# Performance work log

Measured on AMD Instinct MI355X. Metric: run time of the kernel, lower is better.

Reference implementation:

```python
import jax, jax.numpy as jnp
import numpy as np

EPS = 1e-6
E_LAMBDA = 1e-4
HID = 128


def conv1d_same(z, w, b):
    # z: [B,C,S], w: [O,I,K] -> [B,O,S]
    out = jax.lax.conv_general_dilated(z, w, window_strides=(1,), padding='SAME',
                                       dimension_numbers=('NCH', 'OIH', 'NCH'))
    return out + b[None, :, None]


def queue_layer(x, k_s, k_a):
    dist = x[:, :, -3]
    air = x[:, :, -5]
    E_S = k_s * dist + EPS
    lam = k_a / (air + EPS)
    rho = jnp.minimum(lam * E_S, 0.99)  # torch.clamp(max=0.99)
    W_q = rho / (1.0 - rho + EPS) * E_S
    Wn = (W_q - W_q.min()) / (W_q.max() - W_q.min() + EPS)
    L_q = lam * W_q
    Ln = (L_q - L_q.min()) / (L_q.max() - L_q.min() + EPS)
    return Wn[..., None], Ln[..., None]  # [B,S,1] each


def simam(z, d, l):
    # z: [B,C,S]; d,l: [B,1,1]
    mu = z.mean(axis=2, keepdims=True)
    e = ((z - mu) ** 2).mean(axis=2, keepdims=True) + d + 0.5 * l + E_LAMBDA
    return z * jax.nn.sigmoid(e)


def mogrifier_lstm(seq, d_seq, lq_seq, mod_w, mod_b, w_ih, w_hh, b_ih, b_hh):
    # seq: [B,S,C]; d_seq,lq_seq: [B,S,1]
    B = seq.shape[0]
    h0 = jnp.zeros((B, HID), seq.dtype)
    c0 = jnp.zeros((B, HID), seq.dtype)
    xs = (jnp.swapaxes(seq, 0, 1), jnp.swapaxes(d_seq, 0, 1), jnp.swapaxes(lq_seq, 0, 1))

    def step(carry, xt):
        h, c = carry
        s_t, d_t, l_t = xt
        gate_in = jnp.concatenate([h, d_t, l_t], axis=1)  # [B, H+2]
        m = jax.nn.sigmoid(gate_in @ mod_w.T + mod_b)      # [B, C]
        g = (m * s_t) @ w_ih.T + b_ih + h @ w_hh.T + b_hh  # [B, 4H]
        i, f, gg, o = jnp.split(g, 4, axis=1)              # torch LSTMCell gate order
        c = jax.nn.sigmoid(f) * c + jax.nn.sigmoid(i) * jnp.tanh(gg)
        h = jax.nn.sigmoid(o) * jnp.tanh(c)
        return (h, c), None

    (h, _), _ = jax.lax.scan(step, (h0, c0), xs)
    return h


def setup_inputs() -> dict:
    key = jax.random.key(0)
    ks = jax.random.split(key, 16)
    s = 0.02
    B, S, F = 256, 512, 16
    C1, C2, C3, H, NC = 64, 128, 256, HID, 8
    inp = {
        'x': jax.random.uniform(ks[0], (B, S, F), dtype=jnp.float32),
        'k_s': jnp.float32(1.0),
        'k_a': jnp.float32(1.0),
        'w1': jax.random.normal(ks[1], (C1, F, 3), jnp.float32) * s,
        'b1': jnp.zeros((C1,), jnp.float32),
        'w2': jax.random.normal(ks[2], (C2, C1, 3), jnp.float32) * s,
        'b2': jnp.zeros((C2,), jnp.float32),
        'w3': jax.random.normal(ks[3], (C3, C2, 3), jnp.float32) * s,
        'b3': jnp.zeros((C3,), jnp.float32),
        'mod_w': jax.random.normal(ks[4], (C3, H + 2), jnp.float32) * s,
        'mod_b': jnp.zeros((C3,), jnp.float32),
        'w_ih': jax.random.normal(ks[5], (4 * H, C3), jnp.float32) * s,
        'w_hh': jax.random.normal(ks[6], (4 * H, H), jnp.float32) * s,
        'b_ih': jnp.zeros((4 * H,), jnp.float32),
        'b_hh': jnp.zeros((4 * H,), jnp.float32),
        'cls_w': jax.random.normal(ks[7], (NC, H), jnp.float32) * s,
        'cls_b': jnp.zeros((NC,), jnp.float32),
    }
    return inp


def reference(x, k_s, k_a, w1, b1, w2, b2, w3, b3, mod_w, mod_b,
              w_ih, w_hh, b_ih, b_hh, cls_w, cls_b):
    d_seq, lq_seq = queue_layer(x, k_s, k_a)       # [B,S,1] each
    d = d_seq.mean(axis=1, keepdims=True).transpose(0, 2, 1)   # [B,1,1]
    l = lq_seq.mean(axis=1, keepdims=True).transpose(0, 2, 1)  # [B,1,1]
    z = x.transpose(0, 2, 1)                       # [B,F,S]
    for w, b in ((w1, b1), (w2, b2), (w3, b3)):
        z = simam(jax.nn.relu(conv1d_same(z, w, b)), d, l)
    z = z.transpose(0, 2, 1)                       # [B,S,C3]
    h_last = mogrifier_lstm(z, d_seq, lq_seq, mod_w, mod_b, w_ih, w_hh, b_ih, b_hh)
    return h_last @ cls_w.T + cls_b                # [B,num_classes]
```

## Files before the change

kernel.cpp:

```cpp
#include <hip/hip_runtime.h>
#include <hip/hip_fp16.h>
#include <cstdint>

#define EPSQ 1e-6f
#define E_LAM 1e-4f

#define B_ 256
#define S_ 512
#define F_ 16
#define C1_ 64
#define C2_ 128
#define C3_ 256
#define HID_ 128

typedef _Float16 f16x8 __attribute__((ext_vector_type(8)));
typedef _Float16 f16x4 __attribute__((ext_vector_type(4)));
typedef float f32x4 __attribute__((ext_vector_type(4)));

__device__ __forceinline__ float sigm(float x){
  return __builtin_amdgcn_rcpf(1.0f + __builtin_amdgcn_exp2f(-1.44269504f*x));
}
__device__ __forceinline__ float tanhft(float x){
  float e = __builtin_amdgcn_exp2f(-2.88539008f*x);
  return (1.0f - e) * __builtin_amdgcn_rcpf(1.0f + e);
}

#define PINV(x) asm volatile("" : "+v"(reinterpret_cast<f32x4&>(x)))

__global__ void k_init(unsigned int* mm){
  int t = threadIdx.x;
  if (t < 4) mm[t] = (t & 1) ? 0u : 0x7f800000u;
}

__global__ __launch_bounds__(256) void k_queue1(
    const float* __restrict__ x, const float* __restrict__ ksp, const float* __restrict__ kap,
    float* __restrict__ Wq, float* __restrict__ Lq, unsigned int* __restrict__ mm){
  int i = blockIdx.x * 256 + threadIdx.x;
  float ks = ksp[0], ka = kap[0];
  float dist = x[(size_t)i*F_ + 13];
  float air  = x[(size_t)i*F_ + 11];
  float ES  = ks*dist + EPSQ;
  float lam = ka/(air + EPSQ);
  float rho = fminf(lam*ES, 0.99f);
  float wq  = rho/(1.0f - rho + EPSQ)*ES;
  float lq  = lam*wq;
  Wq[i] = wq; Lq[i] = lq;
  float wmin=wq, wmax=wq, lmin=lq, lmax=lq;
  for (int o=32;o;o>>=1){
    wmin = fminf(wmin, __shfl_xor(wmin,o));
    wmax = fmaxf(wmax, __shfl_xor(wmax,o));
    lmin = fminf(lmin, __shfl_xor(lmin,o));
    lmax = fmaxf(lmax, __shfl_xor(lmax,o));
  }
  if ((threadIdx.x & 63) == 0){
    atomicMin(mm+0, __float_as_uint(wmin));
    atomicMax(mm+1, __float_as_uint(wmax));
    atomicMin(mm+2, __float_as_uint(lmin));
    atomicMax(mm+3, __float_as_uint(lmax));
  }
}

__global__ __launch_bounds__(256) void k_queue2(
    float* __restrict__ Wq, float* __restrict__ Lq, const unsigned int* __restrict__ mm,
    float* __restrict__ dbar, float* __restrict__ lbar){
  int b = blockIdx.x, t = threadIdx.x;
  float minW = __uint_as_float(mm[0]), maxW = __uint_as_float(mm[1]);
  float minL = __uint_as_float(mm[2]), maxL = __uint_as_float(mm[3]);
  float dW = maxW - minW + EPSQ;
  float dL = maxL - minL + EPSQ;
  float sw = 0.f, sl = 0.f;
  for (int s=t; s<S_; s+=256){
    size_t idx = (size_t)b*S_ + s;
    float wn = (Wq[idx]-minW)/dW;
    float ln = (Lq[idx]-minL)/dL;
    Wq[idx]=wn; Lq[idx]=ln;
    sw += wn; sl += ln;
  }
  for (int o=32;o;o>>=1){ sw += __shfl_xor(sw,o); sl += __shfl_xor(sl,o); }
  __shared__ float rs[4], rl[4];
  int w = t>>6;
  if ((t&63)==0){ rs[w]=sw; rl[w]=sl; }
  __syncthreads();
  if (t==0){
    dbar[b] = (rs[0]+rs[1]+rs[2]+rs[3]) * (1.0f/S_);
    lbar[b] = (rl[0]+rl[1]+rl[2]+rl[3]) * (1.0f/S_);
  }
}

__global__ void k_repack_conv(const float* __restrict__ w, float* __restrict__ wr, int CIN, int COUT){
  int idx = blockIdx.x*256 + threadIdx.x;
  int N = CIN*COUT*3;
  if (idx >= N) return;
  int co = idx % COUT;
  int r  = idx / COUT;
  int k  = r % 3;
  int ci = r / 3;
  wr[idx] = w[((size_t)co*CIN + ci)*3 + k];
}

__global__ void k_repack_w3f(const float* __restrict__ w3, __half* __restrict__ W3f){
  int idx = blockIdx.x*256 + threadIdx.x;
  if (idx >= 98304) return;
  int f = idx & 7, l = (idx>>3) & 63, t = idx >> 9;
  int kb = t % 12, nt = t / 12;
  int co = nt*16 + (l&15);
  int K  = kb*32 + ((l>>4)<<3) + f;
  int kidx = K >> 7, ci = K & 127;
  W3f[idx] = __float2half(w3[((size_t)co*C2_ + ci)*3 + kidx]);
}

__global__ void k_repack_frags(
    const float* __restrict__ mod_w, const float* __restrict__ w_ih, const float* __restrict__ w_hh,
    const float* __restrict__ b_ih, const float* __restrict__ b_hh, const float* __restrict__ mod_b,
    __half* __restrict__ WIHf, __half* __restrict__ WHHf, __half* __restrict__ MWf,
    float* __restrict__ BG){
  int idx = blockIdx.x*256 + threadIdx.x;
  const int NIH = 32*8*512;
  const int NHH = 32*4*512;
  const int NMW = 16*5*512;
  if (idx < NIH){
    int f = idx & 7, l = (idx>>3)&63; int t = idx>>9; int kk = t & 7; int nt = t>>3;
    int row = nt*16 + (l&15), k = kk*32 + ((l>>4)<<3) + f;
    WIHf[idx] = __float2half(w_ih[(size_t)row*256 + k]);
  } else if (idx < NIH+NHH){
    int j = idx - NIH;
    int f = j&7, l = (j>>3)&63; int t = j>>9; int kk = t&3; int nt = t>>2;
    int row = nt*16 + (l&15), k = kk*32 + ((l>>4)<<3) + f;
    WHHf[j] = __float2half(w_hh[(size_t)row*128 + k]);
  } else if (idx < NIH+NHH+NMW){
    int j = idx - NIH - NHH;
    int f = j&7, l = (j>>3)&63; int t = j>>9; int kk = t%5; int nt = t/5;
    int row = nt*16 + (l&15), k = kk*32 + ((l>>4)<<3) + f;
    float v = (k < 130) ? mod_w[(size_t)row*130 + k] : ((k == 130) ? mod_b[row] : 0.0f);
    MWf[j] = __float2half(v);
  } else if (idx < NIH+NHH+NMW+512){
    int k = idx - NIH-NHH-NMW;
    BG[k] = b_ih[k] + b_hh[k];
  }
}

template<int CIN, int COUT, int TOUT>
__global__ __launch_bounds__(256) void k_conv(
    const float* __restrict__ in, const float* __restrict__ wr,
    const float* __restrict__ bias, float* __restrict__ out){
  constexpr int SG    = 256/COUT;
  constexpr int STILE = SG*8;
  constexpr int RS    = STILE+4;
  __shared__ __align__(16) float lds[CIN*RS];
  int b = blockIdx.y;
  int s_base = blockIdx.x * STILE;
  int tid = threadIdx.x;
  for (int idx=tid; idx<CIN*(STILE+2); idx+=256){
    int ci = idx & (F_-1);
    int sp = idx >> 4;
    int sg = s_base - 1 + sp;
    float v = (sg>=0 && sg<S_) ? in[((size_t)b*S_+sg)*F_ + ci] : 0.0f;
    lds[ci*RS+sp] = v;
  }
  __syncthreads();
  int co = tid % COUT;
  int sg = tid / COUT;
  int s0 = sg*8;
  float acc[8] = {0,0,0,0,0,0,0,0};
  for (int ci=0; ci<CIN; ci++){
    const float* w = &wr[(ci*3)*COUT + co];
    float w0=w[0], w1=w[COUT], w2=w[2*COUT];
    const float* r = &lds[ci*RS + s0];
    float4 va = *(const float4*)(r);
    float4 vb = *(const float4*)(r+4);
    float2 vc = *(const float2*)(r+8);
    float v[10] = {va.x,va.y,va.z,va.w, vb.x,vb.y,vb.z,vb.w, vc.x,vc.y};
    #pragma unroll
    for (int ss=0; ss<8; ss++) acc[ss] += w0*v[ss] + w1*v[ss+1] + w2*v[ss+2];
  }
  float bb = bias[co];
  float* o = &out[((size_t)b*COUT+co)*S_ + s_base + s0];
  float4 o0 = make_float4(fmaxf(acc[0]+bb,0.f), fmaxf(acc[1]+bb,0.f), fmaxf(acc[2]+bb,0.f), fmaxf(acc[3]+bb,0.f));
  float4 o1 = make_float4(fmaxf(acc[4]+bb,0.f), fmaxf(acc[5]+bb,0.f), fmaxf(acc[6]+bb,0.f), fmaxf(acc[7]+bb,0.f));
  *(float4*)(o)   = o0;
  *(float4*)(o+4) = o1;
}

template<int CIN, int COUT, int TOUT>
__global__ __launch_bounds__(256) void k_cgemm(
    const float* __restrict__ in, const float* __restrict__ wr,
    const float* __restrict__ bias, const float* __restrict__ gate,
    float* __restrict__ out){
  constexpr int TS   = 64;
  constexpr int RS   = 72;
  constexpr int SPT  = COUT/32;
  constexpr int NCG  = COUT/8;
  constexpr int KC   = (CIN == 64) ? 8 : 4;
  constexpr int WROW = NCG*10;
  __shared__ __align__(16) float sIn[CIN*RS];
  __shared__ __align__(16) float sW[3*KC*WROW];
  int b = blockIdx.y;
  int s_base = blockIdx.x * TS;
  int tid = threadIdx.x;
  for (int idx = tid; idx < CIN*(TS+2); idx += 256){
    int ci = idx / (TS+2), sp = idx % (TS+2);
    int sg = s_base - 1 + sp;
    float v = (sg>=0 && sg<S_) ? in[((size_t)b*CIN+ci)*S_ + sg] : 0.0f;
    sIn[ci*RS + sp] = v * gate[b*CIN + ci];
  }
  int cg = tid % NCG, sg2 = tid / NCG;
  int co0 = cg*8, s0 = sg2*SPT;
  float2 acc[8][SPT/2] = {};
  for (int ci0 = 0; ci0 < CIN; ci0 += KC){
    __syncthreads();
    for (int e = tid; e < 3*KC*COUT; e += 256){
      int krow = e / COUT, co = e % COUT;
      sW[krow*WROW + (co>>3)*10 + (co&7)] = wr[(size_t)3*ci0*COUT + e];
    }
    __syncthreads();
    #pragma unroll
    for (int cii = 0; cii < KC; cii++){
      const float* rp = &sIn[(ci0+cii)*RS + s0];
      float win[SPT+4];
      #pragma unroll
      for (int j = 0; j < (SPT+4)/4; j++)
        *(float4*)&win[4*j] = *(const float4*)(rp + 4*j);
      #pragma unroll
      for (int kidx = 0; kidx < 3; kidx++){
        const float* wrow = &sW[(cii*3 + kidx)*WROW + cg*10];
        float ws[8];
        *(float2*)&ws[0] = *(const float2*)(wrow);
        *(float2*)&ws[2] = *(const float2*)(wrow+2);
        *(float2*)&ws[4] = *(const float2*)(wrow+4);
        *(float2*)&ws[6] = *(const float2*)(wrow+6);
        #pragma unroll
        for (int i = 0; i < 8; i++){
          #pragma unroll
          for (int j = 0; j < SPT/2; j++){
            acc[i][j].x += ws[i]*win[2*j+kidx];
            acc[i][j].y += ws[i]*win[2*j+1+kidx];
          }
        }
      }
    }
  }
  float bs[8];
  *(float4*)&bs[0] = *(const float4*)(bias+co0);
  *(float4*)&bs[4] = *(const float4*)(bias+co0+4);
  #pragma unroll
  for (int i=0;i<8;i++){
    float v[SPT];
    #pragma unroll
    for (int j=0;j<SPT;j++){
      float a = (j&1) ? acc[i][j>>1].y : acc[i][j>>1].x;
      v[j] = fmaxf(a + bs[i], 0.0f);
    }
    float* op = &out[((size_t)b*COUT+co0+i)*S_ + s_base+s0];
    #pragma unroll
    for (int j4=0;j4<SPT;j4+=4) *(float4*)(op+j4) = *(float4*)&v[j4];
  }
}

__global__ __launch_bounds__(256) void k_cmfma3(
    const float* __restrict__ z2, const __half* __restrict__ W3f,
    const float* __restrict__ bias, const float* __restrict__ gate,
    float* __restrict__ out){
  __shared__ __align__(16) _Float16 zT[66*128];
  int b = blockIdx.y;
  int s_base = blockIdx.x * 64;
  int tid = threadIdx.x;
  const int lane = tid & 63, w = tid >> 6;
  for (int idx = tid; idx < 128*66; idx += 256){
    int ci = idx / 66, j = idx % 66;
    int sg = s_base + j - 1;
    float v = (sg >= 0 && sg < S_) ? z2[((size_t)b*C2_ + ci)*S_ + sg] * gate[b*C2_ + ci] : 0.0f;
    *(_Float16*)((char*)zT + ((j*256 + ci*2) ^ ((j&7)<<4))) = (_Float16)v;
  }
  __syncthreads();
  f32x4 acc[4][4];
  float bv[4];
  #pragma unroll
  for (int i=0;i<4;i++) bv[i] = bias[(w*4+i)*16 + (lane&15)];
  #pragma unroll
  for (int ts=0;ts<4;ts++)
    #pragma unroll
    for (int i=0;i<4;i++) acc[ts][i] = (f32x4){bv[i],bv[i],bv[i],bv[i]};

  const f16x8* Bf = (const f16x8*)W3f;
  for (int kb=0; kb<12; kb++){
    f16x8 bfr[4];
    #pragma unroll
    for (int i=0;i<4;i++)
      bfr[i] = Bf[(((w*4+i)*12 + kb)<<6) + lane];
    int colb = ((kb&3)*32 + ((lane>>4)<<3))*2;
    f16x8 afr[4];
    #pragma unroll
    for (int ts=0;ts<4;ts++){
      int row = ts*16 + (lane&15) + (kb>>2);
      afr[ts] = *(const f16x8*)((const char*)zT + ((row*256 + colb) ^ ((row&7)<<4)));
    }
    #pragma unroll
    for (int ts=0;ts<4;ts++)
      #pragma unroll
      for (int i=0;i<4;i++)
        acc[ts][i] = __builtin_amdgcn_mfma_f32_16x16x32_f16(afr[ts], bfr[i], acc[ts][i], 0,0,0);
  }
  #pragma unroll
  for (int ts=0; ts<4; ts++){
    #pragma unroll
    for (int i=0; i<4; i++){
      int co = (w*4+i)*16 + (lane&15);
      #pragma unroll
      for (int r=0;r<4;r++){
        int srow = s_base + ts*16 + ((lane>>4)<<2) + r;
        out[((size_t)b*S_ + srow)*C3_ + co] = fmaxf(acc[ts][i][r], 0.0f);
      }
    }
  }
}

template<int C>
__global__ __launch_bounds__(256) void k_gate(
    const float* __restrict__ z, const float* __restrict__ dbar,
    const float* __restrict__ lbar, float* __restrict__ gate){
  int bid = blockIdx.x;
  int b = bid / C, c = bid % C;
  const float* row = z + ((size_t)b*C + c)*S_;
  int t = threadIdx.x;
  float v0 = row[t], v1 = row[t+256];
  float s = v0+v1, q = v0*v0 + v1*v1;
  for (int o=32;o;o>>=1){ s += __shfl_xor(s,o); q += __shfl_xor(q,o); }
  __shared__ float rs[4], rq[4];
  int w = t>>6;
  if ((t&63)==0){ rs[w]=s; rq[w]=q; }
  __syncthreads();
  if (t==0){
    float st = rs[0]+rs[1]+rs[2]+rs[3];
    float qt = rq[0]+rq[1]+rq[2]+rq[3];
    float mu  = st*(1.0f/S_);
    float var = qt*(1.0f/S_) - mu*mu;
    float e = var + dbar[b] + 0.5f*lbar[b] + E_LAM;
    gate[b*C + c] = 1.0f/(1.0f + expf(-e));
  }
}

__global__ __launch_bounds__(1024) void k_simam2(
    float* __restrict__ zt, const float* __restrict__ dbar, const float* __restrict__ lbar){
  int b = blockIdx.x;
  int tid = threadIdx.x;
  int c = tid & 255, part = tid >> 8;
  float* base = zt + ((size_t)b*S_ + part*128)*C3_ + c;
  float s=0.f, q=0.f;
  #pragma unroll 4
  for (int i=0;i<128;i++){ float v = base[(size_t)i*C3_]; s+=v; q+=v*v; }
  __shared__ float S4[4][256], Q4[4][256], gate[256];
  S4[part][c]=s; Q4[part][c]=q;
  __syncthreads();
  if (part==0){
    float st = S4[0][c]+S4[1][c]+S4[2][c]+S4[3][c];
    float qt = Q4[0][c]+Q4[1][c]+Q4[2][c]+Q4[3][c];
    float mu  = st*(1.0f/S_);
    float var = qt*(1.0f/S_) - mu*mu;
    float e = var + dbar[b] + 0.5f*lbar[b] + E_LAM;
    gate[c] = 1.0f/(1.0f+expf(-e));
  }
  __syncthreads();
  float g = gate[c];
  #pragma unroll 4
  for (int i=0;i<128;i++) base[(size_t)i*C3_] *= g;
}

#define MOG_OFF   0
#define MS_OFF    81920
#define MS_STRIDE 528
#define H_OFF     (MS_OFF + 16*MS_STRIDE)
#define H_STRIDE  272
#define H_BUF     (16*H_STRIDE)
#define BG_OFF    (H_OFF + 2*H_BUF)
#define SMEM_SZ   (BG_OFF + 2048)

__global__ __launch_bounds__(512) __attribute__((amdgpu_waves_per_eu(2, 2)))
void k_lstm_mfma(
    const float* __restrict__ zt, const float* __restrict__ Wn, const float* __restrict__ Ln,
    const __half* __restrict__ WIHf, const __half* __restrict__ WHHf, const __half* __restrict__ MWf,
    const float* __restrict__ BG, const float* __restrict__ cls_w, const float* __restrict__ cls_b,
    float* __restrict__ out){
  __shared__ __align__(16) char smem[SMEM_SZ];
  const int tid = threadIdx.x;
  const int lane = tid & 63, w = tid >> 6;
  const int batch = lane & 15, kq = lane >> 4;
  const int b0 = blockIdx.x * 16;

  {
    const f32x4* src = (const f32x4*)MWf;
    for (int i = tid; i < 5120; i += 512)
      *(f32x4*)(smem + MOG_OFF + (size_t)i*16) = src[i];
    int wq = tid >> 6, rem = tid & 63, kq2 = rem >> 4, j = rem & 15, g = j >> 2, r = j & 3;
    ((float*)(smem + BG_OFF))[tid] = BG[g*128 + wq*16 + kq2*4 + r];
    for (int i = tid; i < 2*H_BUF/4; i += 512)
      ((unsigned int*)(smem + H_OFF))[i] = 0u;
  }

  const f16x8* WIHv = (const f16x8*)WIHf;
  const f16x8* WHHv = (const f16x8*)WHHf;
  f16x8 wihr[8][4];
  #pragma unroll
  for (int kk=0; kk<8; kk++)
    #pragma unroll
    for (int g=0; g<4; g++)
      wihr[kk][g] = WIHv[(((w + g*8)*8 + kk)<<6) + lane];
  f16x8 whr[4][4];
  #pragma unroll
  for (int g=0; g<4; g++)
    #pragma unroll
    for (int kk=0; kk<4; kk++)
      whr[g][kk] = WHHv[(((w + g*8)*4 + kk)<<6) + lane];
  #pragma unroll
  for (int kk=0; kk<8; kk++)
    #pragma unroll
    for (int g=0; g<4; g++) PINV(wihr[kk][g]);
  #pragma unroll
  for (int g=0; g<4; g++)
    #pragma unroll
    for (int kk=0; kk<4; kk++) PINV(whr[g][kk]);

  const float* zb  = zt + (size_t)(b0 + batch)*S_*C3_;
  const float* wnp = Wn + (size_t)(b0 + batch)*S_;
  const float* lnp = Ln + (size_t)(b0 + batch)*S_;

  char*       ms_w0 = smem + MS_OFF + batch*MS_STRIDE + (2*w+0)*32 + kq*8;
  char*       ms_w1 = smem + MS_OFF + batch*MS_STRIDE + (2*w+1)*32 + kq*8;
  const char* ms_rd = smem + MS_OFF + batch*MS_STRIDE + kq*16;
  char*       h_wr  = smem + H_OFF + batch*H_STRIDE + w*32 + kq*8;
  const char* h_rd  = smem + H_OFF + batch*H_STRIDE + kq*16;
  const float* bgp  = (const float*)(smem + BG_OFF) + (w*4 + kq)*16;
  const char* mogp  = smem + MOG_OFF + lane*16;

  f32x4 cst = {0.f,0.f,0.f,0.f};
  f32x4 hv  = {0.f,0.f,0.f,0.f};

  f32x4 zv0c = *(const f32x4*)(zb + (2*w+0)*16 + kq*4);
  f32x4 zv1c = *(const f32x4*)(zb + (2*w+1)*16 + kq*4);
  float dvc = wnp[0], lvc = lnp[0];
  __syncthreads();

  for (int t=0; t<S_; t++){
    const int p = t & 1;
    const char* hrd = h_rd + p*H_BUF;
    f16x8 hb0[4];
    #pragma unroll
    for (int kk=0; kk<4; kk++)
      hb0[kk] = *(const f16x8*)(hrd + kk*64);
    f16x8 dlb = {0,0,0,0,0,0,0,0};
    if (kq == 0){ dlb[0] = (_Float16)dvc; dlb[1] = (_Float16)lvc; dlb[2] = (_Float16)1.0f; }
    f32x4 am0 = {0,0,0,0}, am1 = {0,0,0,0};
    f16x8 mg0 = *(const f16x8*)(mogp + (((2*w+0)*5 + 0)<<10));
    f16x8 mg1 = *(const f16x8*)(mogp + (((2*w+1)*5 + 0)<<10));
    #pragma unroll
    for (int kk=0; kk<5; kk++){
      f16x8 n0, n1;
      if (kk < 4){
        n0 = *(const f16x8*)(mogp + (((2*w+0)*5 + kk+1)<<10));
        n1 = *(const f16x8*)(mogp + (((2*w+1)*5 + kk+1)<<10));
      }
      f16x8 bfr = (kk < 4) ? hb0[kk] : dlb;
      am0 = __builtin_amdgcn_mfma_f32_16x16x32_f16(mg0, bfr, am0, 0,0,0);
      am1 = __builtin_amdgcn_mfma_f32_16x16x32_f16(mg1, bfr, am1, 0,0,0);
      if (kk < 4){ mg0 = n0; mg1 = n1; }
    }
    f16x4 msv;
    #pragma unroll
    for (int r=0;r<4;r++) msv[r] = (_Float16)(sigm(am0[r]) * zv0c[r]);
    *(f16x4*)ms_w0 = msv;
    #pragma unroll
    for (int r=0;r<4;r++) msv[r] = (_Float16)(sigm(am1[r]) * zv1c[r]);
    *(f16x4*)ms_w1 = msv;
    f32x4 acc[4];
    #pragma unroll
    for (int g=0; g<4; g++) acc[g] = *(const f32x4*)(bgp + g*4);
    #pragma unroll
    for (int kk=0; kk<4; kk++){
      #pragma unroll
      for (int g=0; g<4; g++)
        acc[g] = __builtin_amdgcn_mfma_f32_16x16x32_f16(whr[g][kk], hb0[kk], acc[g], 0,0,0);
    }
    __syncthreads();
    int tn = (t+1 < S_) ? t+1 : t;
    zv0c = *(const f32x4*)(zb + (size_t)tn*C3_ + (2*w+0)*16 + kq*4);
    zv1c = *(const f32x4*)(zb + (size_t)tn*C3_ + (2*w+1)*16 + kq*4);
    dvc = wnp[tn]; lvc = lnp[tn];
    f16x8 mscur = *(const f16x8*)(ms_rd);
    #pragma unroll
    for (int kk=0; kk<8; kk++){
      f16x8 msn;
      if (kk < 7) msn = *(const f16x8*)(ms_rd + (kk+1)*64);
      #pragma unroll
      for (int g=0; g<4; g++)
        acc[g] = __builtin_amdgcn_mfma_f32_16x16x32_f16(wihr[kk][g], mscur, acc[g], 0,0,0);
      if (kk < 7) mscur = msn;
    }
    #pragma unroll
    for (int r=0; r<4; r++){
      float cc = sigm(acc[1][r]) * cst[r] + sigm(acc[0][r]) * tanhft(acc[2][r]);
      cst[r] = cc;
      hv[r] = sigm(acc[3][r]) * tanhft(cc);
    }
    f16x4 hp;
    #pragma unroll
    for (int r=0;r<4;r++) hp[r] = (_Float16)hv[r];
    *(f16x4*)(h_wr + (p^1)*H_BUF) = hp;
    __syncthreads();
  }
  *(f32x4*)(smem + MS_OFF + batch*512 + w*64 + kq*16) = hv;
  __syncthreads();
  if (tid < 128){
    int bb = tid >> 3, oo = tid & 7;
    const float* hf = (const float*)(smem + MS_OFF) + bb*128;
    float a = cls_b[oo];
    #pragma unroll 16
    for (int k2=0; k2<HID_; k2++) a += hf[k2]*cls_w[oo*HID_+k2];
    out[(b0+bb)*8 + oo] = a;
  }
}

extern "C" void kernel_launch(void* const* d_in, const int* in_sizes, int n_in,
                              void* d_out, int out_size, void* d_ws, size_t ws_size,
                              hipStream_t stream){
  const float* x     = (const float*)d_in[0];
  const float* k_s   = (const float*)d_in[1];
  const float* k_a   = (const float*)d_in[2];
  const float* w1    = (const float*)d_in[3];
  const float* b1    = (const float*)d_in[4];
  const float* w2    = (const float*)d_in[5];
  const float* b2    = (const float*)d_in[6];
  const float* w3    = (const float*)d_in[7];
  const float* b3    = (const float*)d_in[8];
  const float* mod_w = (const float*)d_in[9];
  const float* mod_b = (const float*)d_in[10];
  const float* w_ih  = (const float*)d_in[11];
  const float* w_hh  = (const float*)d_in[12];
  const float* b_ih  = (const float*)d_in[13];
  const float* b_hh  = (const float*)d_in[14];
  const float* cls_w = (const float*)d_in[15];
  const float* cls_b = (const float*)d_in[16];
  float* outp = (float*)d_out;

  char* ws = (char*)d_ws;
  size_t o = 0;
  auto alloc = [&](size_t bytes){ size_t r = o; o = (o + bytes + 255) & ~(size_t)255; return r; };
  float*        Wq   = (float*)(ws + alloc((size_t)B_*S_*4));
  float*        Lq   = (float*)(ws + alloc((size_t)B_*S_*4));
  unsigned int* MM   = (unsigned int*)(ws + alloc(16));
  float*        DB   = (float*)(ws + alloc(B_*4));
  float*        LB   = (float*)(ws + alloc(B_*4));
  float*        WR1  = (float*)(ws + alloc((size_t)F_*3*C1_*4));
  float*        WR2  = (float*)(ws + alloc((size_t)C1_*3*C2_*4));
  __half*       W3f  = (__half*)(ws + alloc((size_t)98304*2));
  __half*       WIHf = (__half*)(ws + alloc((size_t)32*8*512*2));
  __half*       WHHf = (__half*)(ws + alloc((size_t)32*4*512*2));
  __half*       MWf  = (__half*)(ws + alloc((size_t)16*5*512*2));
  float*        BG   = (float*)(ws + alloc(512*4));
  float*        G1   = (float*)(ws + alloc((size_t)B_*C1_*4));
  float*        G2   = (float*)(ws + alloc((size_t)B_*C2_*4));
  float*        Z1   = (float*)(ws + alloc((size_t)B_*C1_*S_*4));
  float*        Z2   = (float*)(ws + alloc((size_t)B_*C2_*S_*4));
  float*        ZT3  = (float*)(ws + alloc((size_t)B_*S_*C3_*4));
  (void)ws_size; (void)in_sizes; (void)n_in; (void)out_size;

  hipLaunchKernelGGL(k_init, dim3(1), dim3(64), 0, stream, MM);
  hipLaunchKernelGGL(k_queue1, dim3((B_*S_)/256), dim3(256), 0, stream, x, k_s, k_a, Wq, Lq, MM);
  hipLaunchKernelGGL(k_queue2, dim3(B_), dim3(256), 0, stream, Wq, Lq, MM, DB, LB);

  hipLaunchKernelGGL(k_repack_conv, dim3((F_*3*C1_+255)/256), dim3(256), 0, stream, w1, WR1, F_, C1_);
  hipLaunchKernelGGL(k_repack_conv, dim3((C1_*3*C2_+255)/256), dim3(256), 0, stream, w2, WR2, C1_, C2_);
  hipLaunchKernelGGL(k_repack_w3f, dim3((98304+255)/256), dim3(256), 0, stream, w3, W3f);
  {
    int N = 32*8*512 + 32*4*512 + 16*5*512 + 512;
    hipLaunchKernelGGL(k_repack_frags, dim3((N+255)/256), dim3(256), 0, stream,
                       mod_w, w_ih, w_hh, b_ih, b_hh, mod_b, WIHf, WHHf, MWf, BG);
  }

  hipLaunchKernelGGL((k_conv<F_, C1_, 0>), dim3(S_/32, B_), dim3(256), 0, stream, x,  WR1, b1, Z1);
  hipLaunchKernelGGL((k_gate<C1_>), dim3(B_*C1_), dim3(256), 0, stream, Z1, DB, LB, G1);
  hipLaunchKernelGGL((k_cgemm<C1_, C2_, 0>), dim3(S_/64, B_), dim3(256), 0, stream, Z1, WR2, b2, G1, Z2);
  hipLaunchKernelGGL((k_gate<C2_>), dim3(B_*C2_), dim3(256), 0, stream, Z2, DB, LB, G2);
  hipLaunchKernelGGL(k_cmfma3, dim3(S_/64, B_), dim3(256), 0, stream, Z2, W3f, b3, G2, ZT3);
  hipLaunchKernelGGL(k_simam2, dim3(B_), dim3(1024), 0, stream, ZT3, DB, LB);

  hipLaunchKernelGGL(k_lstm_mfma, dim3(B_/16), dim3(512), 0, stream,
                     ZT3, Wq, Lq, WIHf, WHHf, MWf, BG, cls_w, cls_b, outp);
}
```

Measured before the change: 1.518 ms.

## Split LSTM recurrence across 16 waves with register-resident mogrifier weights

The recurrent LSTM kernel now runs 1024 threads (16 waves) per block instead of 512. Each wave handles one 16-channel mogrifier slice and two gate tiles: waves 0-7 compute the i/g gates and waves 8-15 the f/o gates. The high waves pass sigmoid(f) and sigmoid(o) through shared memory to the low waves, which update c and h. Mogrifier weights and biases move from LDS into registers, shortening each wave's serial MFMA chain per timestep at the cost of an extra barrier and extra LDS traffic per step.

```diff
diff --git a/kernel.cpp b/kernel.cpp
--- a/kernel.cpp
+++ b/kernel.cpp
@@ -365,152 +365,154 @@
   for (int i=0;i<128;i++) base[(size_t)i*C3_] *= g;
 }
 
-#define MOG_OFF   0
-#define MS_OFF    81920
-#define MS_STRIDE 528
-#define H_OFF     (MS_OFF + 16*MS_STRIDE)
-#define H_STRIDE  272
-#define H_BUF     (16*H_STRIDE)
-#define BG_OFF    (H_OFF + 2*H_BUF)
-#define SMEM_SZ   (BG_OFF + 2048)
-
-__global__ __launch_bounds__(512) __attribute__((amdgpu_waves_per_eu(2, 2)))
-void k_lstm_mfma(
+#define L2_MS_STRIDE 528
+#define L2_H_OFF     (16*L2_MS_STRIDE)
+#define L2_H_STRIDE  272
+#define L2_H_BUF     (16*L2_H_STRIDE)
+#define L2_SF_OFF    (L2_H_OFF + 2*L2_H_BUF)
+#define L2_SB_STRIDE 528
+#define L2_SO_OFF    (L2_SF_OFF + 16*L2_SB_STRIDE)
+#define L2_SMEM      (L2_SO_OFF + 16*L2_SB_STRIDE)
+
+__global__ __launch_bounds__(1024) __attribute__((amdgpu_waves_per_eu(4, 4)))
+void k_lstm_mfma2(
     const float* __restrict__ zt, const float* __restrict__ Wn, const float* __restrict__ Ln,
     const __half* __restrict__ WIHf, const __half* __restrict__ WHHf, const __half* __restrict__ MWf,
     const float* __restrict__ BG, const float* __restrict__ cls_w, const float* __restrict__ cls_b,
     float* __restrict__ out){
-  __shared__ __align__(16) char smem[SMEM_SZ];
+  __shared__ __align__(16) char smem[L2_SMEM];
   const int tid = threadIdx.x;
   const int lane = tid & 63, w = tid >> 6;
   const int batch = lane & 15, kq = lane >> 4;
   const int b0 = blockIdx.x * 16;
-
-  {
-    const f32x4* src = (const f32x4*)MWf;
-    for (int i = tid; i < 5120; i += 512)
-      *(f32x4*)(smem + MOG_OFF + (size_t)i*16) = src[i];
-    int wq = tid >> 6, rem = tid & 63, kq2 = rem >> 4, j = rem & 15, g = j >> 2, r = j & 3;
-    ((float*)(smem + BG_OFF))[tid] = BG[g*128 + wq*16 + kq2*4 + r];
-    for (int i = tid; i < 2*H_BUF/4; i += 512)
-      ((unsigned int*)(smem + H_OFF))[i] = 0u;
-  }
+  const bool lowg = (w < 8);
 
   const f16x8* WIHv = (const f16x8*)WIHf;
   const f16x8* WHHv = (const f16x8*)WHHf;
-  f16x8 wihr[8][4];
-  #pragma unroll
-  for (int kk=0; kk<8; kk++)
-    #pragma unroll
-    for (int g=0; g<4; g++)
-      wihr[kk][g] = WIHv[(((w + g*8)*8 + kk)<<6) + lane];
-  f16x8 whr[4][4];
-  #pragma unroll
-  for (int g=0; g<4; g++)
+  const f16x8* MWv  = (const f16x8*)MWf;
+  f16x8 wihr[2][8];
+  #pragma unroll
+  for (int t2=0; t2<2; t2++)
+    #pragma unroll
+    for (int kk=0; kk<8; kk++)
+      wihr[t2][kk] = WIHv[((((w + t2*16)*8) + kk)<<6) + lane];
+  f16x8 whr[2][4];
+  #pragma unroll
+  for (int t2=0; t2<2; t2++)
     #pragma unroll
     for (int kk=0; kk<4; kk++)
-      whr[g][kk] = WHHv[(((w + g*8)*4 + kk)<<6) + lane];
-  #pragma unroll
-  for (int kk=0; kk<8; kk++)
-    #pragma unroll
-    for (int g=0; g<4; g++) PINV(wihr[kk][g]);
-  #pragma unroll
-  for (int g=0; g<4; g++)
-    #pragma unroll
-    for (int kk=0; kk<4; kk++) PINV(whr[g][kk]);
+      whr[t2][kk] = WHHv[((((w + t2*16)*4) + kk)<<6) + lane];
+  f16x8 mgr[5];
+  #pragma unroll
+  for (int kk=0; kk<5; kk++)
+    mgr[kk] = MWv[(((w*5) + kk)<<6) + lane];
+  #pragma unroll
+  for (int t2=0; t2<2; t2++){
+    #pragma unroll
+    for (int kk=0; kk<8; kk++) PINV(wihr[t2][kk]);
+    #pragma unroll
+    for (int kk=0; kk<4; kk++) PINV(whr[t2][kk]);
+  }
+  #pragma unroll
+  for (int kk=0; kk<5; kk++) PINV(mgr[kk]);
+
+  f32x4 bgv[2];
+  bgv[0] = *(const f32x4*)(BG + w*16 + kq*4);
+  bgv[1] = *(const f32x4*)(BG + (w+16)*16 + kq*4);
+
+  for (int i=tid; i<2*L2_H_BUF/4; i+=1024)
+    ((unsigned int*)(smem + L2_H_OFF))[i] = 0u;
 
   const float* zb  = zt + (size_t)(b0 + batch)*S_*C3_;
   const float* wnp = Wn + (size_t)(b0 + batch)*S_;
   const float* lnp = Ln + (size_t)(b0 + batch)*S_;
-
-  char*       ms_w0 = smem + MS_OFF + batch*MS_STRIDE + (2*w+0)*32 + kq*8;
-  char*       ms_w1 = smem + MS_OFF + batch*MS_STRIDE + (2*w+1)*32 + kq*8;
-  const char* ms_rd = smem + MS_OFF + batch*MS_STRIDE + kq*16;
-  char*       h_wr  = smem + H_OFF + batch*H_STRIDE + w*32 + kq*8;
-  const char* h_rd  = smem + H_OFF + batch*H_STRIDE + kq*16;
-  const float* bgp  = (const float*)(smem + BG_OFF) + (w*4 + kq)*16;
-  const char* mogp  = smem + MOG_OFF + lane*16;
+  const int c0 = w*16 + kq*4;
+
+  char*       ms_w  = smem + batch*L2_MS_STRIDE + w*32 + kq*8;
+  const char* ms_rd = smem + batch*L2_MS_STRIDE + kq*16;
+  char*       h_wr  = smem + L2_H_OFF + batch*L2_H_STRIDE + w*32 + kq*8;
+  const char* h_rd  = smem + L2_H_OFF + batch*L2_H_STRIDE + kq*16;
+  char*       sf_wr = smem + L2_SF_OFF + batch*L2_SB_STRIDE + ((w-8)*16 + kq*4)*4;
+  char*       so_wr = smem + L2_SO_OFF + batch*L2_SB_STRIDE + ((w-8)*16 + kq*4)*4;
+  const char* sf_rd = smem + L2_SF_OFF + batch*L2_SB_STRIDE + (w*16 + kq*4)*4;
+  const char* so_rd = smem + L2_SO_OFF + batch*L2_SB_STRIDE + (w*16 + kq*4)*4;
 
   f32x4 cst = {0.f,0.f,0.f,0.f};
   f32x4 hv  = {0.f,0.f,0.f,0.f};
 
-  f32x4 zv0c = *(const f32x4*)(zb + (2*w+0)*16 + kq*4);
-  f32x4 zv1c = *(const f32x4*)(zb + (2*w+1)*16 + kq*4);
+  f32x4 zvc = *(const f32x4*)(zb + c0);
   float dvc = wnp[0], lvc = lnp[0];
   __syncthreads();
 
   for (int t=0; t<S_; t++){
     const int p = t & 1;
-    const char* hrd = h_rd + p*H_BUF;
+    const char* hrd = h_rd + p*L2_H_BUF;
     f16x8 hb0[4];
     #pragma unroll
     for (int kk=0; kk<4; kk++)
       hb0[kk] = *(const f16x8*)(hrd + kk*64);
     f16x8 dlb = {0,0,0,0,0,0,0,0};
     if (kq == 0){ dlb[0] = (_Float16)dvc; dlb[1] = (_Float16)lvc; dlb[2] = (_Float16)1.0f; }
-    f32x4 am0 = {0,0,0,0}, am1 = {0,0,0,0};
-    f16x8 mg0 = *(const f16x8*)(mogp + (((2*w+0)*5 + 0)<<10));
-    f16x8 mg1 = *(const f16x8*)(mogp + (((2*w+1)*5 + 0)<<10));
-    #pragma unroll
-    for (int kk=0; kk<5; kk++){
-      f16x8 n0, n1;
-      if (kk < 4){
-        n0 = *(const f16x8*)(mogp + (((2*w+0)*5 + kk+1)<<10));
-        n1 = *(const f16x8*)(mogp + (((2*w+1)*5 + kk+1)<<10));
-      }
-      f16x8 bfr = (kk < 4) ? hb0[kk] : dlb;
-      am0 = __builtin_amdgcn_mfma_f32_16x16x32_f16(mg0, bfr, am0, 0,0,0);
-      am1 = __builtin_amdgcn_mfma_f32_16x16x32_f16(mg1, bfr, am1, 0,0,0);
-      if (kk < 4){ mg0 = n0; mg1 = n1; }
-    }
+    f32x4 am = {0,0,0,0};
+    #pragma unroll
+    for (int kk=0; kk<4; kk++)
+      am = __builtin_amdgcn_mfma_f32_16x16x32_f16(mgr[kk], hb0[kk], am, 0,0,0);
+    am = __builtin_amdgcn_mfma_f32_16x16x32_f16(mgr[4], dlb, am, 0,0,0);
     f16x4 msv;
     #pragma unroll
-    for (int r=0;r<4;r++) msv[r] = (_Float16)(sigm(am0[r]) * zv0c[r]);
-    *(f16x4*)ms_w0 = msv;
-    #pragma unroll
-    for (int r=0;r<4;r++) msv[r] = (_Float16)(sigm(am1[r]) * zv1c[r]);
-    *(f16x4*)ms_w1 = msv;
-    f32x4 acc[4];
-    #pragma unroll
-    for (int g=0; g<4; g++) acc[g] = *(const f32x4*)(bgp + g*4);
+    for (int r=0;r<4;r++) msv[r] = (_Float16)(sigm(am[r]) * zvc[r]);
+    *(f16x4*)ms_w = msv;
+    f32x4 acc[2];
+    acc[0] = bgv[0]; acc[1] = bgv[1];
     #pragma unroll
     for (int kk=0; kk<4; kk++){
-      #pragma unroll
-      for (int g=0; g<4; g++)
-        acc[g] = __builtin_amdgcn_mfma_f32_16x16x32_f16(whr[g][kk], hb0[kk], acc[g], 0,0,0);
+      acc[0] = __builtin_amdgcn_mfma_f32_16x16x32_f16(whr[0][kk], hb0[kk], acc[0], 0,0,0);
+      acc[1] = __builtin_amdgcn_mfma_f32_16x16x32_f16(whr[1][kk], hb0[kk], acc[1], 0,0,0);
     }
     __syncthreads();
     int tn = (t+1 < S_) ? t+1 : t;
-    zv0c = *(const f32x4*)(zb + (size_t)tn*C3_ + (2*w+0)*16 + kq*4);
-    zv1c = *(const f32x4*)(zb + (size_t)tn*C3_ + (2*w+1)*16 + kq*4);
+    zvc = *(const f32x4*)(zb + (size_t)tn*C3_ + c0);
     dvc = wnp[tn]; lvc = lnp[tn];
     f16x8 mscur = *(const f16x8*)(ms_rd);
     #pragma unroll
     for (int kk=0; kk<8; kk++){
       f16x8 msn;
       if (kk < 7) msn = *(const f16x8*)(ms_rd + (kk+1)*64);
+      acc[0] = __builtin_amdgcn_mfma_f32_16x16x32_f16(wihr[0][kk], mscur, acc[0], 0,0,0);
+      acc[1] = __builtin_amdgcn_mfma_f32_16x16x32_f16(wihr[1][kk], mscur, acc[1], 0,0,0);
+      if (kk < 7) mscur = msn;
+    }
+    if (!lowg){
+      f32x4 sf, so;
       #pragma unroll
-      for (int g=0; g<4; g++)
-        acc[g] = __builtin_amdgcn_mfma_f32_16x16x32_f16(wihr[kk][g], mscur, acc[g], 0,0,0);
-      if (kk < 7) mscur = msn;
-    }
-    #pragma unroll
-    for (int r=0; r<4; r++){
-      float cc = sigm(acc[1][r]) * cst[r] + sigm(acc[0][r]) * tanhft(acc[2][r]);
-      cst[r] = cc;
-      hv[r] = sigm(acc[3][r]) * tanhft(cc);
-    }
-    f16x4 hp;
-    #pragma unroll
-    for (int r=0;r<4;r++) hp[r] = (_Float16)hv[r];
-    *(f16x4*)(h_wr + (p^1)*H_BUF) = hp;
+      for (int r=0;r<4;r++){ sf[r] = sigm(acc[0][r]); so[r] = sigm(acc[1][r]); }
+      *(f32x4*)sf_wr = sf;
+      *(f32x4*)so_wr = so;
+    }
     __syncthreads();
-  }
-  *(f32x4*)(smem + MS_OFF + batch*512 + w*64 + kq*16) = hv;
+    if (lowg){
+      f32x4 sf = *(const f32x4*)sf_rd;
+      f32x4 so = *(const f32x4*)so_rd;
+      f16x4 hp;
+      #pragma unroll
+      for (int r=0; r<4; r++){
+        float si = sigm(acc[0][r]);
+        float tg = tanhft(acc[1][r]);
+        float cc = sf[r]*cst[r] + si*tg;
+        cst[r] = cc;
+        float hh = so[r]*tanhft(cc);
+        hv[r] = hh;
+        hp[r] = (_Float16)hh;
+      }
+      *(f16x4*)(h_wr + (p^1)*L2_H_BUF) = hp;
+    }
+    __syncthreads();
+  }
+  if (lowg) *(f32x4*)(smem + batch*512 + w*64 + kq*16) = hv;
   __syncthreads();
   if (tid < 128){
     int bb = tid >> 3, oo = tid & 7;
-    const float* hf = (const float*)(smem + MS_OFF) + bb*128;
+    const float* hf = (const float*)smem + bb*128;
     float a = cls_b[oo];
     #pragma unroll 16
     for (int k2=0; k2<HID_; k2++) a += hf[k2]*cls_w[oo*HID_+k2];
@@ -582,6 +584,6 @@
   hipLaunchKernelGGL(k_cmfma3, dim3(S_/64, B_), dim3(256), 0, stream, Z2, W3f, b3, G2, ZT3);
   hipLaunchKernelGGL(k_simam2, dim3(B_), dim3(1024), 0, stream, ZT3, DB, LB);
 
-  hipLaunchKernelGGL(k_lstm_mfma, dim3(B_/16), dim3(512), 0, stream,
+  hipLaunchKernelGGL(k_lstm_mfma2, dim3(B_/16), dim3(1024), 0, stream,
                      ZT3, Wq, Lq, WIHf, WHHf, MWf, BG, cls_w, cls_b, outp);
 }
```

Result: slower. 4.309 ms (+183.8%).

## Replace FP32 conv2 register-tiled GEMM with FP16 MFMA kernel

Applied to the files above, without the earlier changes.

The second convolution (64->128 channels, kernel width 3) moves from an FP32 register-tiled implicit GEMM onto 16x16x32 f16 MFMA instructions. It mirrors the existing conv3 MFMA kernel, using an XOR-swizzled transposed FP16 input tile in LDS and weights pre-packed into fragment order by a new repack kernel. This targets the FP32 FMA cost of conv2, at the price of FP16 rounding of the gated activations and weights.

```diff
diff --git a/kernel.cpp b/kernel.cpp
--- a/kernel.cpp
+++ b/kernel.cpp
@@ -96,6 +96,17 @@
   int k  = r % 3;
   int ci = r / 3;
   wr[idx] = w[((size_t)co*CIN + ci)*3 + k];
+}
+
+__global__ void k_repack_w2f(const float* __restrict__ w2, __half* __restrict__ W2f){
+  int idx = blockIdx.x*256 + threadIdx.x;
+  if (idx >= 24576) return;
+  int f = idx & 7, l = (idx>>3) & 63, t = idx >> 9;
+  int kb = t % 6, nt = t / 6;
+  int co = nt*16 + (l&15);
+  int K  = kb*32 + ((l>>4)<<3) + f;
+  int kidx = K >> 6, ci = K & 63;
+  W2f[idx] = __float2half(w2[((size_t)co*C1_ + ci)*3 + kidx]);
 }
 
 __global__ void k_repack_w3f(const float* __restrict__ w3, __half* __restrict__ W3f){
@@ -181,78 +192,60 @@
   *(float4*)(o+4) = o1;
 }
 
-template<int CIN, int COUT, int TOUT>
-__global__ __launch_bounds__(256) void k_cgemm(
-    const float* __restrict__ in, const float* __restrict__ wr,
+__global__ __launch_bounds__(256) void k_cmfma2(
+    const float* __restrict__ z1, const __half* __restrict__ W2f,
     const float* __restrict__ bias, const float* __restrict__ gate,
     float* __restrict__ out){
-  constexpr int TS   = 64;
-  constexpr int RS   = 72;
-  constexpr int SPT  = COUT/32;
-  constexpr int NCG  = COUT/8;
-  constexpr int KC   = (CIN == 64) ? 8 : 4;
-  constexpr int WROW = NCG*10;
-  __shared__ __align__(16) float sIn[CIN*RS];
-  __shared__ __align__(16) float sW[3*KC*WROW];
+  __shared__ __align__(16) _Float16 zT1[66*64];
   int b = blockIdx.y;
-  int s_base = blockIdx.x * TS;
+  int s_base = blockIdx.x * 64;
   int tid = threadIdx.x;
-  for (int idx = tid; idx < CIN*(TS+2); idx += 256){
-    int ci = idx / (TS+2), sp = idx % (TS+2);
-    int sg = s_base - 1 + sp;
-    float v = (sg>=0 && sg<S_) ? in[((size_t)b*CIN+ci)*S_ + sg] : 0.0f;
-    sIn[ci*RS + sp] = v * gate[b*CIN + ci];
-  }
-  int cg = tid % NCG, sg2 = tid / NCG;
-  int co0 = cg*8, s0 = sg2*SPT;
-  float2 acc[8][SPT/2] = {};
-  for (int ci0 = 0; ci0 < CIN; ci0 += KC){
-    __syncthreads();
-    for (int e = tid; e < 3*KC*COUT; e += 256){
-      int krow = e / COUT, co = e % COUT;
-      sW[krow*WROW + (co>>3)*10 + (co&7)] = wr[(size_t)3*ci0*COUT + e];
-    }
-    __syncthreads();
-    #pragma unroll
-    for (int cii = 0; cii < KC; cii++){
-      const float* rp = &sIn[(ci0+cii)*RS + s0];
-      float win[SPT+4];
+  const int lane = tid & 63, w = tid >> 6;
+  for (int idx = tid; idx < 64*66; idx += 256){
+    int ci = idx / 66, j = idx % 66;
+    int sg = s_base + j - 1;
+    float v = (sg >= 0 && sg < S_) ? z1[((size_t)b*C1_ + ci)*S_ + sg] * gate[b*C1_ + ci] : 0.0f;
+    *(_Float16*)((char*)zT1 + ((j*128 + ci*2) ^ ((j&7)<<4))) = (_Float16)v;
+  }
+  __syncthreads();
+  f32x4 acc[4][2];
+  float bv[2];
+  #pragma unroll
+  for (int i=0;i<2;i++) bv[i] = bias[(w*2+i)*16 + (lane&15)];
+  #pragma unroll
+  for (int ts=0;ts<4;ts++)
+    #pragma unroll
+    for (int i=0;i<2;i++) acc[ts][i] = (f32x4){bv[i],bv[i],bv[i],bv[i]};
+
+  const f16x8* Bf = (const f16x8*)W2f;
+  for (int kb=0; kb<6; kb++){
+    f16x8 bfr[2];
+    #pragma unroll
+    for (int i=0;i<2;i++)
+      bfr[i] = Bf[(((w*2+i)*6 + kb)<<6) + lane];
+    int colb = ((kb&1)*32 + ((lane>>4)<<3))*2;
+    f16x8 afr[4];
+    #pragma unroll
+    for (int ts=0;ts<4;ts++){
+      int row = ts*16 + (lane&15) + (kb>>1);
+      afr[ts] = *(const f16x8*)((const char*)zT1 + ((row*128 + colb) ^ ((row&7)<<4)));
+    }
+    #pragma unroll
+    for (int ts=0;ts<4;ts++)
       #pragma unroll
-      for (int j = 0; j < (SPT+4)/4; j++)
-        *(float4*)&win[4*j] = *(const float4*)(rp + 4*j);
-      #pragma unroll
-      for (int kidx = 0; kidx < 3; kidx++){
-        const float* wrow = &sW[(cii*3 + kidx)*WROW + cg*10];
-        float ws[8];
-        *(float2*)&ws[0] = *(const float2*)(wrow);
-        *(float2*)&ws[2] = *(const float2*)(wrow+2);
-        *(float2*)&ws[4] = *(const float2*)(wrow+4);
-        *(float2*)&ws[6] = *(const float2*)(wrow+6);
-        #pragma unroll
-        for (int i = 0; i < 8; i++){
-          #pragma unroll
-          for (int j = 0; j < SPT/2; j++){
-            acc[i][j].x += ws[i]*win[2*j+kidx];
-            acc[i][j].y += ws[i]*win[2*j+1+kidx];
-          }
-        }
-      }
-    }
-  }
-  float bs[8];
-  *(float4*)&bs[0] = *(const float4*)(bias+co0);
-  *(float4*)&bs[4] = *(const float4*)(bias+co0+4);
-  #pragma unroll
-  for (int i=0;i<8;i++){
-    float v[SPT];
-    #pragma unroll
-    for (int j=0;j<SPT;j++){
-      float a = (j&1) ? acc[i][j>>1].y : acc[i][j>>1].x;
-      v[j] = fmaxf(a + bs[i], 0.0f);
-    }
-    float* op = &out[((size_t)b*COUT+co0+i)*S_ + s_base+s0];
-    #pragma unroll
-    for (int j4=0;j4<SPT;j4+=4) *(float4*)(op+j4) = *(float4*)&v[j4];
+      for (int i=0;i<2;i++)
+        acc[ts][i] = __builtin_amdgcn_mfma_f32_16x16x32_f16(afr[ts], bfr[i], acc[ts][i], 0,0,0);
+  }
+  #pragma unroll
+  for (int ts=0; ts<4; ts++){
+    #pragma unroll
+    for (int i=0; i<2; i++){
+      int co = (w*2+i)*16 + (lane&15);
+      int srow = s_base + ts*16 + ((lane>>4)<<2);
+      float4 v4 = make_float4(fmaxf(acc[ts][i][0],0.f), fmaxf(acc[ts][i][1],0.f),
+                              fmaxf(acc[ts][i][2],0.f), fmaxf(acc[ts][i][3],0.f));
+      *(float4*)&out[((size_t)b*C2_ + co)*S_ + srow] = v4;
+    }
   }
 }
 
@@ -549,7 +542,7 @@
   float*        DB   = (float*)(ws + alloc(B_*4));
   float*        LB   = (float*)(ws + alloc(B_*4));
   float*        WR1  = (float*)(ws + alloc((size_t)F_*3*C1_*4));
-  float*        WR2  = (float*)(ws + alloc((size_t)C1_*3*C2_*4));
+  __half*       W2f  = (__half*)(ws + alloc((size_t)24576*2));
   __half*       W3f  = (__half*)(ws + alloc((size_t)98304*2));
   __half*       WIHf = (__half*)(ws + alloc((size_t)32*8*512*2));
   __half*       WHHf = (__half*)(ws + alloc((size_t)32*4*512*2));
@@ -567,7 +560,7 @@
   hipLaunchKernelGGL(k_queue2, dim3(B_), dim3(256), 0, stream, Wq, Lq, MM, DB, LB);
 
   hipLaunchKernelGGL(k_repack_conv, dim3((F_*3*C1_+255)/256), dim3(256), 0, stream, w1, WR1, F_, C1_);
-  hipLaunchKernelGGL(k_repack_conv, dim3((C1_*3*C2_+255)/256), dim3(256), 0, stream, w2, WR2, C1_, C2_);
+  hipLaunchKernelGGL(k_repack_w2f, dim3((24576+255)/256), dim3(256), 0, stream, w2, W2f);
   hipLaunchKernelGGL(k_repack_w3f, dim3((98304+255)/256), dim3(256), 0, stream, w3, W3f);
   {
     int N = 32*8*512 + 32*4*512 + 16*5*512 + 512;
@@ -577,7 +570,7 @@
 
   hipLaunchKernelGGL((k_conv<F_, C1_, 0>), dim3(S_/32, B_), dim3(256), 0, stream, x,  WR1, b1, Z1);
   hipLaunchKernelGGL((k_gate<C1_>), dim3(B_*C1_), dim3(256), 0, stream, Z1, DB, LB, G1);
-  hipLaunchKernelGGL((k_cgemm<C1_, C2_, 0>), dim3(S_/64, B_), dim3(256), 0, stream, Z1, WR2, b2, G1, Z2);
+  hipLaunchKernelGGL(k_cmfma2, dim3(S_/64, B_), dim3(256), 0, stream, Z1, W2f, b2, G1, Z2);
   hipLaunchKernelGGL((k_gate<C2_>), dim3(B_*C2_), dim3(256), 0, stream, Z2, DB, LB, G2);
   hipLaunchKernelGGL(k_cmfma3, dim3(S_/64, B_), dim3(256), 0, stream, Z2, W3f, b3, G2, ZT3);
   hipLaunchKernelGGL(k_simam2, dim3(B_), dim3(1024), 0, stream, ZT3, DB, LB);
```

After: 1.391 ms. 1.09x faster.
